# Optimization experiments

Measured on AMD Instinct MI355X. Metric: run time of the kernel, lower is better.

The kernel has to match this reference:

```python
import jax, jax.numpy as jnp
import numpy as np

N, E = 50000, 800000
IN_DIM, HEADS, OUT_DIM = 128, 4, 32
NEG_SLOPE = 0.2
EPS = 1e-16


def setup_inputs() -> dict:
    key = jax.random.key(0)
    k = jax.random.split(key, 6)
    x = jax.random.normal(k[0], (N, IN_DIM), dtype=jnp.float32)
    edge_index = jax.random.randint(k[1], (2, E), 0, N, dtype=jnp.int64)
    # xavier-uniform-ish params
    lim_w = float(np.sqrt(6.0 / (IN_DIM + HEADS * OUT_DIM)))
    W = jax.random.uniform(k[2], (HEADS * OUT_DIM, IN_DIM), minval=-lim_w, maxval=lim_w, dtype=jnp.float32)
    lim_a = float(np.sqrt(6.0 / (1 + HEADS * OUT_DIM)))
    att_src = jax.random.uniform(k[3], (1, HEADS, OUT_DIM), minval=-lim_a, maxval=lim_a, dtype=jnp.float32)
    att_dst = jax.random.uniform(k[4], (1, HEADS, OUT_DIM), minval=-lim_a, maxval=lim_a, dtype=jnp.float32)
    bias = jnp.zeros((HEADS * OUT_DIM,), dtype=jnp.float32)
    return {"x": x, "edge_index": edge_index, "W": W, "att_src": att_src, "att_dst": att_dst, "bias": bias}


def reference(x, edge_index, W, att_src, att_dst, bias):
    n = x.shape[0]
    h = (x @ W.T).reshape(n, HEADS, OUT_DIM)           # (N,H,D)
    src, dst = edge_index[0], edge_index[1]
    a_src = jnp.sum(h * att_src, axis=-1)              # (N,H)
    a_dst = jnp.sum(h * att_dst, axis=-1)              # (N,H)
    alpha = a_src[src] + a_dst[dst]                    # (E,H)
    alpha = jax.nn.leaky_relu(alpha, NEG_SLOPE)
    # segment (per-dst) softmax over edges, per head
    m = jax.ops.segment_max(alpha, dst, num_segments=n)   # (N,H)
    ex = jnp.exp(alpha - m[dst])
    s = jax.ops.segment_sum(ex, dst, num_segments=n)      # (N,H)
    alpha = ex / (s[dst] + EPS)                            # (E,H)
    # dropout p=0 (eval) -> identity
    msg = h[src] * alpha[..., None]                        # (E,H,D)
    out = jax.ops.segment_sum(msg, dst, num_segments=n)    # (N,H,D)
    out = out.reshape(n, HEADS * OUT_DIM) + bias
    alpha_pooled = alpha.mean(axis=-1)                     # (E,)
    return out, alpha_pooled
```

## Files before the change

### kernel.cpp

```cpp
#include <hip/hip_runtime.h>

#define NNODES 50000
#define NEDGES 800000
#define HD 128
#define NEG 0.2f
#define MTILE 64
#define LDW 136
#define MAXD 64
#define GEMMB ((NNODES + MTILE - 1) / MTILE)
#define NBINS 196
#define CAP 5120
#define GST 16
#define ABLK ((NEDGES + 2047) / 2048)

typedef __attribute__((ext_vector_type(8))) short short8;
typedef __attribute__((ext_vector_type(4))) float floatx4;

static __device__ inline unsigned short f2bf(float f) {
    unsigned u = __float_as_uint(f);
    return (unsigned short)((u + 0x7FFF + ((u >> 16) & 1)) >> 16);
}
static __device__ inline float bf2f(unsigned short u) {
    return __uint_as_float(((unsigned)u) << 16);
}
static __device__ inline float lrelu_exp(float a) {
    a = (a > 0.f) ? a : NEG * a;
    return __expf(a);
}

__global__ __launch_bounds__(256, 4) void gat_main(
    const float* __restrict__ x, const float* __restrict__ W,
    const float* __restrict__ att_src, const float* __restrict__ att_dst,
    const int* __restrict__ ei,
    unsigned short* __restrict__ h, float* __restrict__ asrc,
    float* __restrict__ adst, int* __restrict__ gcnt, int2* __restrict__ cbuf)
{
    __shared__ unsigned short Wl[128 * LDW];
    const int t = threadIdx.x;

    if (blockIdx.x >= GEMMB) {
        int* hist = (int*)Wl;
        int* boff = hist + 256;
        const int e0 = (blockIdx.x - GEMMB) * 2048 + t * 8;
        const bool act = (e0 < NEDGES);
        int4 s0 = make_int4(0, 0, 0, 0), s1 = s0, d0 = s0, d1 = s0;
        if (act) {
            s0 = *(const int4*)(ei + e0);
            s1 = *(const int4*)(ei + e0 + 4);
            d0 = *(const int4*)(ei + NEDGES + e0);
            d1 = *(const int4*)(ei + NEDGES + e0 + 4);
        }
        hist[t] = 0;
        __syncthreads();
        if (act) {
            atomicAdd(&hist[d0.x >> 8], 1); atomicAdd(&hist[d0.y >> 8], 1);
            atomicAdd(&hist[d0.z >> 8], 1); atomicAdd(&hist[d0.w >> 8], 1);
            atomicAdd(&hist[d1.x >> 8], 1); atomicAdd(&hist[d1.y >> 8], 1);
            atomicAdd(&hist[d1.z >> 8], 1); atomicAdd(&hist[d1.w >> 8], 1);
        }
        __syncthreads();
        if (t < NBINS && hist[t] > 0)
            boff[t] = atomicAdd(&gcnt[t * GST], hist[t]);
        __syncthreads();
        if (act) {
            int ss[8] = {s0.x, s0.y, s0.z, s0.w, s1.x, s1.y, s1.z, s1.w};
            int dd[8] = {d0.x, d0.y, d0.z, d0.w, d1.x, d1.y, d1.z, d1.w};
#pragma unroll
            for (int j = 0; j < 8; j++) {
                int b = dd[j] >> 8;
                int slot = atomicAdd(&boff[b], 1);
                cbuf[(size_t)b * CAP + slot] =
                    make_int2(((dd[j] & 255) << 16) | ss[j], e0 + j);
            }
        }
        return;
    }

    const int rowBase = blockIdx.x * MTILE;

    for (int idx = t * 8; idx < 128 * 128; idx += 2048) {
        int r = idx >> 7, c = idx & 127;
        float4 v0 = *(const float4*)(W + idx);
        float4 v1 = *(const float4*)(W + idx + 4);
        short8 u;
        u[0] = (short)f2bf(v0.x); u[1] = (short)f2bf(v0.y);
        u[2] = (short)f2bf(v0.z); u[3] = (short)f2bf(v0.w);
        u[4] = (short)f2bf(v1.x); u[5] = (short)f2bf(v1.y);
        u[6] = (short)f2bf(v1.z); u[7] = (short)f2bf(v1.w);
        *(short8*)(Wl + r * LDW + c) = u;
    }

    const int wave = t >> 6;
    const int lane = t & 63;
    const int c16  = lane & 15;
    const int quad = lane >> 4;
    const int xr   = rowBase + wave * 16 + c16;
    short8 av[4];
#pragma unroll
    for (int kc = 0; kc < 4; kc++) {
        float4 v0 = make_float4(0.f, 0.f, 0.f, 0.f);
        float4 v1 = v0;
        if (xr < NNODES) {
            const float* p = x + (size_t)xr * 128 + kc * 32 + quad * 8;
            v0 = *(const float4*)p;
            v1 = *(const float4*)(p + 4);
        }
        short8 u;
        u[0] = (short)f2bf(v0.x); u[1] = (short)f2bf(v0.y);
        u[2] = (short)f2bf(v0.z); u[3] = (short)f2bf(v0.w);
        u[4] = (short)f2bf(v1.x); u[5] = (short)f2bf(v1.y);
        u[6] = (short)f2bf(v1.z); u[7] = (short)f2bf(v1.w);
        av[kc] = u;
    }
    __syncthreads();

    floatx4 acc[8];
#pragma unroll
    for (int nt = 0; nt < 8; nt++) acc[nt] = (floatx4)(0.f);

#pragma unroll
    for (int kc = 0; kc < 4; kc++) {
#pragma unroll
        for (int nt = 0; nt < 8; nt++) {
            short8 bv = *(const short8*)(Wl + (nt * 16 + c16) * LDW + kc * 32 + quad * 8);
            acc[nt] = __builtin_amdgcn_mfma_f32_16x16x32_bf16(av[kc], bv, acc[nt], 0, 0, 0);
        }
    }

    float As[8], Ad[8];
#pragma unroll
    for (int nt = 0; nt < 8; nt++) {
        As[nt] = att_src[nt * 16 + c16];
        Ad[nt] = att_dst[nt * 16 + c16];
    }
#pragma unroll
    for (int r = 0; r < 4; r++) {
        const int gr = rowBase + wave * 16 + quad * 4 + r;
#pragma unroll
        for (int hh = 0; hh < 4; hh++) {
            float ps = acc[2 * hh][r] * As[2 * hh] + acc[2 * hh + 1][r] * As[2 * hh + 1];
            float pd = acc[2 * hh][r] * Ad[2 * hh] + acc[2 * hh + 1][r] * Ad[2 * hh + 1];
#pragma unroll
            for (int m = 8; m >= 1; m >>= 1) {
                ps += __shfl_xor(ps, m, 64);
                pd += __shfl_xor(pd, m, 64);
            }
            if (c16 == 0 && gr < NNODES) {
                asrc[gr * 4 + hh] = ps;
                adst[gr * 4 + hh] = pd;
            }
        }
    }

    __syncthreads();
#pragma unroll
    for (int r = 0; r < 4; r++) {
        const int lr = wave * 16 + quad * 4 + r;
#pragma unroll
        for (int nt = 0; nt < 8; nt++)
            Wl[lr * LDW + nt * 16 + c16] = f2bf(acc[nt][r]);
    }
    __syncthreads();
    for (int idx = t * 8; idx < MTILE * 128; idx += 2048) {
        int r = idx >> 7, c = idx & 127;
        int g = rowBase + r;
        if (g < NNODES)
            *(short8*)(h + (size_t)g * HD + c) = *(const short8*)(Wl + r * LDW + c);
    }
}

__global__ __launch_bounds__(1024) void gat_bin(
    const int* __restrict__ gcnt, const int2* __restrict__ cbuf,
    int* __restrict__ coff, int2* __restrict__ csr)
{
    __shared__ int sh[256];
    __shared__ int hist[256];
    const int t = threadIdx.x;
    const int b = blockIdx.x;
    const int c_b = gcnt[b * GST];

    int v = 0;
    if (t < 256) {
        v = (t < NBINS) ? gcnt[t * GST] : 0;
        sh[t] = v;
        hist[t] = 0;
    }
    __syncthreads();
    for (int off = 1; off < 256; off <<= 1) {
        int u = (t < 256 && t >= off) ? sh[t - off] : 0;
        __syncthreads();
        if (t < 256) sh[t] += u;
        __syncthreads();
    }
    const int binbase = sh[b] - c_b;

    for (int i = t; i < c_b; i += 1024)
        atomicAdd(&hist[(cbuf[(size_t)b * CAP + i].x >> 16) & 255], 1);
    __syncthreads();

    int hv = 0;
    if (t < 256) { hv = hist[t]; sh[t] = hv; }
    __syncthreads();
    for (int off = 1; off < 256; off <<= 1) {
        int u = (t < 256 && t >= off) ? sh[t - off] : 0;
        __syncthreads();
        if (t < 256) sh[t] += u;
        __syncthreads();
    }
    if (t < 256) {
        int ex = sh[t] - hv;
        int n = b * 256 + t;
        if (n < NNODES) coff[n] = binbase + ex;
        hist[t] = ex;
    }
    if (b == 0 && t == 0) coff[NNODES] = NEDGES;
    __syncthreads();

    for (int i = t; i < c_b; i += 1024) {
        int2 ew = cbuf[(size_t)b * CAP + i];
        int fine = (ew.x >> 16) & 255;
        int slot = atomicAdd(&hist[fine], 1);
        csr[binbase + slot] = make_int2(ew.x & 0xffff, ew.y);
    }
}

__global__ __launch_bounds__(256) void gat_node(
    const int* __restrict__ coff, const int2* __restrict__ csr_se,
    const float* __restrict__ asrc, const float* __restrict__ adst,
    const unsigned short* __restrict__ h, const float* __restrict__ bias,
    float* __restrict__ out, float* __restrict__ apool)
{
    __shared__ int   sh_src[8 * MAXD];
    __shared__ int   sh_eid[8 * MAXD];
    __shared__ float sh_w[8 * MAXD * 4];
    int t = threadIdx.x;
    int node8 = t >> 5;
    int n = blockIdx.x * 8 + node8;
    int k = t & 31;
    int head = k >> 3;
    int beg = coff[n], end = coff[n + 1];
    const float4 bn = *(const float4*)(adst + n * 4);

    float4 sum = make_float4(0.f, 0.f, 0.f, 0.f);
    for (int j = beg + k; j < end; j += 32) {
        int2 se = csr_se[j];
        float4 a = *(const float4*)(asrc + se.x * 4);
        float4 wv;
        wv.x = lrelu_exp(a.x + bn.x);
        wv.y = lrelu_exp(a.y + bn.y);
        wv.z = lrelu_exp(a.z + bn.z);
        wv.w = lrelu_exp(a.w + bn.w);
        sum.x += wv.x; sum.y += wv.y; sum.z += wv.z; sum.w += wv.w;
        int i = j - beg;
        if (i < MAXD) {
            sh_src[node8 * MAXD + i] = se.x;
            sh_eid[node8 * MAXD + i] = se.y;
            *(float4*)(sh_w + (node8 * MAXD + i) * 4) = wv;
        }
    }
#pragma unroll
    for (int m = 16; m >= 1; m >>= 1) {
        sum.x += __shfl_xor(sum.x, m, 64);
        sum.y += __shfl_xor(sum.y, m, 64);
        sum.z += __shfl_xor(sum.z, m, 64);
        sum.w += __shfl_xor(sum.w, m, 64);
    }
    float rs[4];
    rs[0] = 1.f / (sum.x + 1e-16f);
    rs[1] = 1.f / (sum.y + 1e-16f);
    rs[2] = 1.f / (sum.z + 1e-16f);
    rs[3] = 1.f / (sum.w + 1e-16f);
    const float rsel = rs[head];
    __syncthreads();

    const int cnt = end - beg;
    const int lim = (cnt < MAXD) ? cnt : MAXD;
    const int base = node8 * MAXD;
    float4 acc = *(const float4*)(bias + k * 4);
    float4 acc2 = make_float4(0.f, 0.f, 0.f, 0.f);
    int i = 0;
    for (; i + 4 <= lim; i += 4) {
        int s0 = sh_src[base + i];
        int s1 = sh_src[base + i + 1];
        int s2 = sh_src[base + i + 2];
        int s3 = sh_src[base + i + 3];
        float w0 = sh_w[(base + i) * 4 + head] * rsel;
        float w1 = sh_w[(base + i + 1) * 4 + head] * rsel;
        float w2 = sh_w[(base + i + 2) * 4 + head] * rsel;
        float w3 = sh_w[(base + i + 3) * 4 + head] * rsel;
        ushort4 u0 = *(const ushort4*)(h + (size_t)s0 * HD + k * 4);
        ushort4 u1 = *(const ushort4*)(h + (size_t)s1 * HD + k * 4);
        ushort4 u2 = *(const ushort4*)(h + (size_t)s2 * HD + k * 4);
        ushort4 u3 = *(const ushort4*)(h + (size_t)s3 * HD + k * 4);
        acc.x  = fmaf(bf2f(u0.x), w0, acc.x);
        acc.y  = fmaf(bf2f(u0.y), w0, acc.y);
        acc.z  = fmaf(bf2f(u0.z), w0, acc.z);
        acc.w  = fmaf(bf2f(u0.w), w0, acc.w);
        acc2.x = fmaf(bf2f(u1.x), w1, acc2.x);
        acc2.y = fmaf(bf2f(u1.y), w1, acc2.y);
        acc2.z = fmaf(bf2f(u1.z), w1, acc2.z);
        acc2.w = fmaf(bf2f(u1.w), w1, acc2.w);
        acc.x  = fmaf(bf2f(u2.x), w2, acc.x);
        acc.y  = fmaf(bf2f(u2.y), w2, acc.y);
        acc.z  = fmaf(bf2f(u2.z), w2, acc.z);
        acc.w  = fmaf(bf2f(u2.w), w2, acc.w);
        acc2.x = fmaf(bf2f(u3.x), w3, acc2.x);
        acc2.y = fmaf(bf2f(u3.y), w3, acc2.y);
        acc2.z = fmaf(bf2f(u3.z), w3, acc2.z);
        acc2.w = fmaf(bf2f(u3.w), w3, acc2.w);
    }
    for (; i < lim; i++) {
        int s0 = sh_src[base + i];
        float w0 = sh_w[(base + i) * 4 + head] * rsel;
        ushort4 u0 = *(const ushort4*)(h + (size_t)s0 * HD + k * 4);
        acc.x = fmaf(bf2f(u0.x), w0, acc.x);
        acc.y = fmaf(bf2f(u0.y), w0, acc.y);
        acc.z = fmaf(bf2f(u0.z), w0, acc.z);
        acc.w = fmaf(bf2f(u0.w), w0, acc.w);
    }
    for (int j = beg + MAXD; j < end; j++) {
        int2 se = csr_se[j];
        float4 a = *(const float4*)(asrc + se.x * 4);
        float w4[4];
        w4[0] = lrelu_exp(a.x + bn.x);
        w4[1] = lrelu_exp(a.y + bn.y);
        w4[2] = lrelu_exp(a.z + bn.z);
        w4[3] = lrelu_exp(a.w + bn.w);
        float w0 = w4[head] * rsel;
        ushort4 u0 = *(const ushort4*)(h + (size_t)se.x * HD + k * 4);
        acc.x = fmaf(bf2f(u0.x), w0, acc.x);
        acc.y = fmaf(bf2f(u0.y), w0, acc.y);
        acc.z = fmaf(bf2f(u0.z), w0, acc.z);
        acc.w = fmaf(bf2f(u0.w), w0, acc.w);
        if (k == 0)
            apool[se.y] = 0.25f * (w4[0] * rs[0] + w4[1] * rs[1] +
                                   w4[2] * rs[2] + w4[3] * rs[3]);
    }
    acc.x += acc2.x; acc.y += acc2.y; acc.z += acc2.z; acc.w += acc2.w;
    *(float4*)(out + (size_t)n * HD + k * 4) = acc;

    for (int i2 = k; i2 < lim; i2 += 32) {
        float4 w = *(const float4*)(sh_w + (base + i2) * 4);
        apool[sh_eid[base + i2]] =
            0.25f * (w.x * rs[0] + w.y * rs[1] + w.z * rs[2] + w.w * rs[3]);
    }
}

extern "C" void kernel_launch(void* const* d_in, const int* in_sizes, int n_in,
                              void* d_out, int out_size, void* d_ws, size_t ws_size,
                              hipStream_t stream)
{
    const float* x       = (const float*)d_in[0];
    const int*   ei      = (const int*)d_in[1];
    const float* W       = (const float*)d_in[2];
    const float* att_src = (const float*)d_in[3];
    const float* att_dst = (const float*)d_in[4];
    const float* bias    = (const float*)d_in[5];

    float* out   = (float*)d_out;
    float* apool = out + (size_t)NNODES * HD;

    unsigned short* h = (unsigned short*)d_ws;
    float* asrc = (float*)(h + (size_t)NNODES * HD);
    float* adst = asrc + NNODES * 4;
    int*   gcnt = (int*)(adst + NNODES * 4);
    int*   coff = gcnt + NBINS * GST;
    int2*  cbuf = (int2*)(coff + NNODES + 4);
    int2*  csr  = cbuf + (size_t)NBINS * CAP;

    hipMemsetAsync(gcnt, 0, (size_t)NBINS * GST * sizeof(int), stream);

    gat_main<<<GEMMB + ABLK, 256, 0, stream>>>(
        x, W, att_src, att_dst, ei, h, asrc, adst, gcnt, cbuf);
    gat_bin<<<NBINS, 1024, 0, stream>>>(gcnt, cbuf, coff, csr);
    gat_node<<<NNODES / 8, 256, 0, stream>>>(
        coff, csr, asrc, adst, h, bias, out, apool);
}
```

Before: 157.6 us.

## Fuse CSR bin sort into node aggregation and compute alpha pooling per edge

Removes the separate gat_bin kernel and global CSR array. Each fused block now re-reads its coarse bin bucket, sorts the 64 destination nodes it owns into shared memory, and aggregates directly from there. The pooled attention output moves to a new edge-parallel kernel that recomputes each edge's weight from saved per-node reciprocal sums, so edge ids no longer need to be stored. The coarse bucket payload shrinks to one int per edge. Each bucket is now scanned by four blocks, the new kernel adds a pass over the edges, and edges past ECAP per quarter bin are silently dropped.

After: 166.5 us. +5.6%, slower.

```diff
diff --git a/kernel.cpp b/kernel.cpp
--- a/kernel.cpp
+++ b/kernel.cpp
@@ -6,12 +6,12 @@
 #define NEG 0.2f
 #define MTILE 64
 #define LDW 136
-#define MAXD 64
 #define GEMMB ((NNODES + MTILE - 1) / MTILE)
 #define NBINS 196
 #define CAP 5120
 #define GST 16
 #define ABLK ((NEDGES + 2047) / 2048)
+#define ECAP 1536
 
 typedef __attribute__((ext_vector_type(8))) short short8;
 typedef __attribute__((ext_vector_type(4))) float floatx4;
@@ -33,7 +33,7 @@
     const float* __restrict__ att_src, const float* __restrict__ att_dst,
     const int* __restrict__ ei,
     unsigned short* __restrict__ h, float* __restrict__ asrc,
-    float* __restrict__ adst, int* __restrict__ gcnt, int2* __restrict__ cbuf)
+    float* __restrict__ adst, int* __restrict__ gcnt, int* __restrict__ cbuf)
 {
     __shared__ unsigned short Wl[128 * LDW];
     const int t = threadIdx.x;
@@ -69,8 +69,7 @@
             for (int j = 0; j < 8; j++) {
                 int b = dd[j] >> 8;
                 int slot = atomicAdd(&boff[b], 1);
-                cbuf[(size_t)b * CAP + slot] =
-                    make_int2(((dd[j] & 255) << 16) | ss[j], e0 + j);
+                cbuf[(size_t)b * CAP + slot] = ((dd[j] & 255) << 16) | ss[j];
             }
         }
         return;
@@ -169,181 +168,171 @@
     }
 }
 
-__global__ __launch_bounds__(1024) void gat_bin(
-    const int* __restrict__ gcnt, const int2* __restrict__ cbuf,
-    int* __restrict__ coff, int2* __restrict__ csr)
-{
-    __shared__ int sh[256];
-    __shared__ int hist[256];
-    const int t = threadIdx.x;
-    const int b = blockIdx.x;
-    const int c_b = gcnt[b * GST];
-
-    int v = 0;
-    if (t < 256) {
-        v = (t < NBINS) ? gcnt[t * GST] : 0;
-        sh[t] = v;
-        hist[t] = 0;
-    }
-    __syncthreads();
-    for (int off = 1; off < 256; off <<= 1) {
-        int u = (t < 256 && t >= off) ? sh[t - off] : 0;
-        __syncthreads();
-        if (t < 256) sh[t] += u;
-        __syncthreads();
-    }
-    const int binbase = sh[b] - c_b;
-
-    for (int i = t; i < c_b; i += 1024)
-        atomicAdd(&hist[(cbuf[(size_t)b * CAP + i].x >> 16) & 255], 1);
-    __syncthreads();
-
-    int hv = 0;
-    if (t < 256) { hv = hist[t]; sh[t] = hv; }
-    __syncthreads();
-    for (int off = 1; off < 256; off <<= 1) {
-        int u = (t < 256 && t >= off) ? sh[t - off] : 0;
-        __syncthreads();
-        if (t < 256) sh[t] += u;
-        __syncthreads();
-    }
-    if (t < 256) {
-        int ex = sh[t] - hv;
-        int n = b * 256 + t;
-        if (n < NNODES) coff[n] = binbase + ex;
-        hist[t] = ex;
-    }
-    if (b == 0 && t == 0) coff[NNODES] = NEDGES;
-    __syncthreads();
-
-    for (int i = t; i < c_b; i += 1024) {
-        int2 ew = cbuf[(size_t)b * CAP + i];
-        int fine = (ew.x >> 16) & 255;
-        int slot = atomicAdd(&hist[fine], 1);
-        csr[binbase + slot] = make_int2(ew.x & 0xffff, ew.y);
-    }
-}
-
-__global__ __launch_bounds__(256) void gat_node(
-    const int* __restrict__ coff, const int2* __restrict__ csr_se,
+__global__ __launch_bounds__(256) void gat_fuse(
+    const int* __restrict__ gcnt, const int* __restrict__ cbuf,
     const float* __restrict__ asrc, const float* __restrict__ adst,
     const unsigned short* __restrict__ h, const float* __restrict__ bias,
-    float* __restrict__ out, float* __restrict__ apool)
-{
-    __shared__ int   sh_src[8 * MAXD];
-    __shared__ int   sh_eid[8 * MAXD];
-    __shared__ float sh_w[8 * MAXD * 4];
-    int t = threadIdx.x;
-    int node8 = t >> 5;
-    int n = blockIdx.x * 8 + node8;
-    int k = t & 31;
-    int head = k >> 3;
-    int beg = coff[n], end = coff[n + 1];
-    const float4 bn = *(const float4*)(adst + n * 4);
-
-    float4 sum = make_float4(0.f, 0.f, 0.f, 0.f);
-    for (int j = beg + k; j < end; j += 32) {
-        int2 se = csr_se[j];
-        float4 a = *(const float4*)(asrc + se.x * 4);
-        float4 wv;
-        wv.x = lrelu_exp(a.x + bn.x);
-        wv.y = lrelu_exp(a.y + bn.y);
-        wv.z = lrelu_exp(a.z + bn.z);
-        wv.w = lrelu_exp(a.w + bn.w);
-        sum.x += wv.x; sum.y += wv.y; sum.z += wv.z; sum.w += wv.w;
-        int i = j - beg;
-        if (i < MAXD) {
-            sh_src[node8 * MAXD + i] = se.x;
-            sh_eid[node8 * MAXD + i] = se.y;
-            *(float4*)(sh_w + (node8 * MAXD + i) * 4) = wv;
-        }
-    }
-#pragma unroll
-    for (int m = 16; m >= 1; m >>= 1) {
-        sum.x += __shfl_xor(sum.x, m, 64);
-        sum.y += __shfl_xor(sum.y, m, 64);
-        sum.z += __shfl_xor(sum.z, m, 64);
-        sum.w += __shfl_xor(sum.w, m, 64);
-    }
-    float rs[4];
-    rs[0] = 1.f / (sum.x + 1e-16f);
-    rs[1] = 1.f / (sum.y + 1e-16f);
-    rs[2] = 1.f / (sum.z + 1e-16f);
-    rs[3] = 1.f / (sum.w + 1e-16f);
-    const float rsel = rs[head];
-    __syncthreads();
-
-    const int cnt = end - beg;
-    const int lim = (cnt < MAXD) ? cnt : MAXD;
-    const int base = node8 * MAXD;
-    float4 acc = *(const float4*)(bias + k * 4);
-    float4 acc2 = make_float4(0.f, 0.f, 0.f, 0.f);
-    int i = 0;
-    for (; i + 4 <= lim; i += 4) {
-        int s0 = sh_src[base + i];
-        int s1 = sh_src[base + i + 1];
-        int s2 = sh_src[base + i + 2];
-        int s3 = sh_src[base + i + 3];
-        float w0 = sh_w[(base + i) * 4 + head] * rsel;
-        float w1 = sh_w[(base + i + 1) * 4 + head] * rsel;
-        float w2 = sh_w[(base + i + 2) * 4 + head] * rsel;
-        float w3 = sh_w[(base + i + 3) * 4 + head] * rsel;
-        ushort4 u0 = *(const ushort4*)(h + (size_t)s0 * HD + k * 4);
-        ushort4 u1 = *(const ushort4*)(h + (size_t)s1 * HD + k * 4);
-        ushort4 u2 = *(const ushort4*)(h + (size_t)s2 * HD + k * 4);
-        ushort4 u3 = *(const ushort4*)(h + (size_t)s3 * HD + k * 4);
-        acc.x  = fmaf(bf2f(u0.x), w0, acc.x);
-        acc.y  = fmaf(bf2f(u0.y), w0, acc.y);
-        acc.z  = fmaf(bf2f(u0.z), w0, acc.z);
-        acc.w  = fmaf(bf2f(u0.w), w0, acc.w);
-        acc2.x = fmaf(bf2f(u1.x), w1, acc2.x);
-        acc2.y = fmaf(bf2f(u1.y), w1, acc2.y);
-        acc2.z = fmaf(bf2f(u1.z), w1, acc2.z);
-        acc2.w = fmaf(bf2f(u1.w), w1, acc2.w);
-        acc.x  = fmaf(bf2f(u2.x), w2, acc.x);
-        acc.y  = fmaf(bf2f(u2.y), w2, acc.y);
-        acc.z  = fmaf(bf2f(u2.z), w2, acc.z);
-        acc.w  = fmaf(bf2f(u2.w), w2, acc.w);
-        acc2.x = fmaf(bf2f(u3.x), w3, acc2.x);
-        acc2.y = fmaf(bf2f(u3.y), w3, acc2.y);
-        acc2.z = fmaf(bf2f(u3.z), w3, acc2.z);
-        acc2.w = fmaf(bf2f(u3.w), w3, acc2.w);
-    }
-    for (; i < lim; i++) {
-        int s0 = sh_src[base + i];
-        float w0 = sh_w[(base + i) * 4 + head] * rsel;
-        ushort4 u0 = *(const ushort4*)(h + (size_t)s0 * HD + k * 4);
-        acc.x = fmaf(bf2f(u0.x), w0, acc.x);
-        acc.y = fmaf(bf2f(u0.y), w0, acc.y);
-        acc.z = fmaf(bf2f(u0.z), w0, acc.z);
-        acc.w = fmaf(bf2f(u0.w), w0, acc.w);
-    }
-    for (int j = beg + MAXD; j < end; j++) {
-        int2 se = csr_se[j];
-        float4 a = *(const float4*)(asrc + se.x * 4);
-        float w4[4];
-        w4[0] = lrelu_exp(a.x + bn.x);
-        w4[1] = lrelu_exp(a.y + bn.y);
-        w4[2] = lrelu_exp(a.z + bn.z);
-        w4[3] = lrelu_exp(a.w + bn.w);
-        float w0 = w4[head] * rsel;
-        ushort4 u0 = *(const ushort4*)(h + (size_t)se.x * HD + k * 4);
-        acc.x = fmaf(bf2f(u0.x), w0, acc.x);
-        acc.y = fmaf(bf2f(u0.y), w0, acc.y);
-        acc.z = fmaf(bf2f(u0.z), w0, acc.z);
-        acc.w = fmaf(bf2f(u0.w), w0, acc.w);
-        if (k == 0)
-            apool[se.y] = 0.25f * (w4[0] * rs[0] + w4[1] * rs[1] +
-                                   w4[2] * rs[2] + w4[3] * rs[3]);
-    }
-    acc.x += acc2.x; acc.y += acc2.y; acc.z += acc2.z; acc.w += acc2.w;
-    *(float4*)(out + (size_t)n * HD + k * 4) = acc;
-
-    for (int i2 = k; i2 < lim; i2 += 32) {
-        float4 w = *(const float4*)(sh_w + (base + i2) * 4);
-        apool[sh_eid[base + i2]] =
-            0.25f * (w.x * rs[0] + w.y * rs[1] + w.z * rs[2] + w.w * rs[3]);
-    }
+    float* __restrict__ out, float* __restrict__ rsumr)
+{
+    __shared__ unsigned short eb[ECAP];
+    __shared__ float sh_w[ECAP * 4];
+    __shared__ int hist[64], run[64], beg[65];
+    const int t = threadIdx.x;
+    const int b = blockIdx.x >> 2;
+    const int q = blockIdx.x & 3;
+    const int c_b = gcnt[b * GST];
+    const size_t wbase = (size_t)b * CAP;
+
+    if (t < 64) hist[t] = 0;
+    __syncthreads();
+    for (int i = t; i < c_b; i += 256) {
+        int e = cbuf[wbase + i];
+        int f = (e >> 16) & 255;
+        if ((f >> 6) == q) atomicAdd(&hist[f & 63], 1);
+    }
+    __syncthreads();
+    if (t < 64) {
+        int v = hist[t];
+        int s = v;
+#pragma unroll
+        for (int off = 1; off < 64; off <<= 1) {
+            int u = __shfl_up(s, off, 64);
+            if (t >= off) s += u;
+        }
+        beg[t] = s - v;
+        run[t] = s - v;
+        if (t == 63) beg[64] = s;
+    }
+    __syncthreads();
+    for (int i = t; i < c_b; i += 256) {
+        int e = cbuf[wbase + i];
+        int f = (e >> 16) & 255;
+        if ((f >> 6) == q) {
+            int slot = atomicAdd(&run[f & 63], 1);
+            if (slot < ECAP) eb[slot] = (unsigned short)(e & 0xFFFF);
+        }
+    }
+    __syncthreads();
+
+    const int grp  = t >> 5;
+    const int k    = t & 31;
+    const int head = k >> 3;
+    const float4 bias4 = *(const float4*)(bias + k * 4);
+
+    for (int ii = 0; ii < 8; ii++) {
+        const int local = grp * 8 + ii;
+        const int n = b * 256 + q * 64 + local;
+        int eB = beg[local], eE = beg[local + 1];
+        if (eE > ECAP) eE = ECAP;
+        if (eB > ECAP) eB = ECAP;
+
+        float4 bn = make_float4(0.f, 0.f, 0.f, 0.f);
+        if (n < NNODES) bn = *(const float4*)(adst + n * 4);
+
+        float4 sum = make_float4(0.f, 0.f, 0.f, 0.f);
+        for (int j = eB + k; j < eE; j += 32) {
+            int s = eb[j];
+            float4 a = *(const float4*)(asrc + s * 4);
+            float4 wv;
+            wv.x = lrelu_exp(a.x + bn.x);
+            wv.y = lrelu_exp(a.y + bn.y);
+            wv.z = lrelu_exp(a.z + bn.z);
+            wv.w = lrelu_exp(a.w + bn.w);
+            sum.x += wv.x; sum.y += wv.y; sum.z += wv.z; sum.w += wv.w;
+            *(float4*)(sh_w + j * 4) = wv;
+        }
+#pragma unroll
+        for (int m = 16; m >= 1; m >>= 1) {
+            sum.x += __shfl_xor(sum.x, m, 64);
+            sum.y += __shfl_xor(sum.y, m, 64);
+            sum.z += __shfl_xor(sum.z, m, 64);
+            sum.w += __shfl_xor(sum.w, m, 64);
+        }
+        float rs[4];
+        rs[0] = 1.f / (sum.x + 1e-16f);
+        rs[1] = 1.f / (sum.y + 1e-16f);
+        rs[2] = 1.f / (sum.z + 1e-16f);
+        rs[3] = 1.f / (sum.w + 1e-16f);
+        if (n < NNODES && k == 0) {
+            float4 r4 = make_float4(rs[0], rs[1], rs[2], rs[3]);
+            *(float4*)(rsumr + n * 4) = r4;
+        }
+        const float rsel = rs[head];
+
+        float4 acc = bias4;
+        float4 acc2 = make_float4(0.f, 0.f, 0.f, 0.f);
+        int i = eB;
+        for (; i + 4 <= eE; i += 4) {
+            int s0 = eb[i];
+            int s1 = eb[i + 1];
+            int s2 = eb[i + 2];
+            int s3 = eb[i + 3];
+            float w0 = sh_w[i * 4 + head] * rsel;
+            float w1 = sh_w[(i + 1) * 4 + head] * rsel;
+            float w2 = sh_w[(i + 2) * 4 + head] * rsel;
+            float w3 = sh_w[(i + 3) * 4 + head] * rsel;
+            ushort4 u0 = *(const ushort4*)(h + (size_t)s0 * HD + k * 4);
+            ushort4 u1 = *(const ushort4*)(h + (size_t)s1 * HD + k * 4);
+            ushort4 u2 = *(const ushort4*)(h + (size_t)s2 * HD + k * 4);
+            ushort4 u3 = *(const ushort4*)(h + (size_t)s3 * HD + k * 4);
+            acc.x  = fmaf(bf2f(u0.x), w0, acc.x);
+            acc.y  = fmaf(bf2f(u0.y), w0, acc.y);
+            acc.z  = fmaf(bf2f(u0.z), w0, acc.z);
+            acc.w  = fmaf(bf2f(u0.w), w0, acc.w);
+            acc2.x = fmaf(bf2f(u1.x), w1, acc2.x);
+            acc2.y = fmaf(bf2f(u1.y), w1, acc2.y);
+            acc2.z = fmaf(bf2f(u1.z), w1, acc2.z);
+            acc2.w = fmaf(bf2f(u1.w), w1, acc2.w);
+            acc.x  = fmaf(bf2f(u2.x), w2, acc.x);
+            acc.y  = fmaf(bf2f(u2.y), w2, acc.y);
+            acc.z  = fmaf(bf2f(u2.z), w2, acc.z);
+            acc.w  = fmaf(bf2f(u2.w), w2, acc.w);
+            acc2.x = fmaf(bf2f(u3.x), w3, acc2.x);
+            acc2.y = fmaf(bf2f(u3.y), w3, acc2.y);
+            acc2.z = fmaf(bf2f(u3.z), w3, acc2.z);
+            acc2.w = fmaf(bf2f(u3.w), w3, acc2.w);
+        }
+        for (; i < eE; i++) {
+            int s0 = eb[i];
+            float w0 = sh_w[i * 4 + head] * rsel;
+            ushort4 u0 = *(const ushort4*)(h + (size_t)s0 * HD + k * 4);
+            acc.x = fmaf(bf2f(u0.x), w0, acc.x);
+            acc.y = fmaf(bf2f(u0.y), w0, acc.y);
+            acc.z = fmaf(bf2f(u0.z), w0, acc.z);
+            acc.w = fmaf(bf2f(u0.w), w0, acc.w);
+        }
+        acc.x += acc2.x; acc.y += acc2.y; acc.z += acc2.z; acc.w += acc2.w;
+        if (n < NNODES)
+            *(float4*)(out + (size_t)n * HD + k * 4) = acc;
+    }
+}
+
+static __device__ inline float apool1(
+    int s, int d, const float* __restrict__ asrc,
+    const float* __restrict__ adst, const float* __restrict__ rsumr)
+{
+    float4 a = *(const float4*)(asrc + s * 4);
+    float4 b = *(const float4*)(adst + d * 4);
+    float4 r = *(const float4*)(rsumr + d * 4);
+    return 0.25f * (lrelu_exp(a.x + b.x) * r.x + lrelu_exp(a.y + b.y) * r.y +
+                    lrelu_exp(a.z + b.z) * r.z + lrelu_exp(a.w + b.w) * r.w);
+}
+
+__global__ __launch_bounds__(256) void gat_apool(
+    const int* __restrict__ ei, const float* __restrict__ asrc,
+    const float* __restrict__ adst, const float* __restrict__ rsumr,
+    float* __restrict__ apool)
+{
+    int e0 = (blockIdx.x * 256 + threadIdx.x) * 4;
+    if (e0 >= NEDGES) return;
+    int4 s = *(const int4*)(ei + e0);
+    int4 d = *(const int4*)(ei + NEDGES + e0);
+    float4 r;
+    r.x = apool1(s.x, d.x, asrc, adst, rsumr);
+    r.y = apool1(s.y, d.y, asrc, adst, rsumr);
+    r.z = apool1(s.z, d.z, asrc, adst, rsumr);
+    r.w = apool1(s.w, d.w, asrc, adst, rsumr);
+    *(float4*)(apool + e0) = r;
 }
 
 extern "C" void kernel_launch(void* const* d_in, const int* in_sizes, int n_in,
@@ -361,18 +350,18 @@
     float* apool = out + (size_t)NNODES * HD;
 
     unsigned short* h = (unsigned short*)d_ws;
-    float* asrc = (float*)(h + (size_t)NNODES * HD);
-    float* adst = asrc + NNODES * 4;
-    int*   gcnt = (int*)(adst + NNODES * 4);
-    int*   coff = gcnt + NBINS * GST;
-    int2*  cbuf = (int2*)(coff + NNODES + 4);
-    int2*  csr  = cbuf + (size_t)NBINS * CAP;
+    float* asrc  = (float*)(h + (size_t)NNODES * HD);
+    float* adst  = asrc + NNODES * 4;
+    float* rsumr = adst + NNODES * 4;
+    int*   gcnt  = (int*)(rsumr + NNODES * 4);
+    int*   cbuf  = gcnt + NBINS * GST;
 
     hipMemsetAsync(gcnt, 0, (size_t)NBINS * GST * sizeof(int), stream);
 
     gat_main<<<GEMMB + ABLK, 256, 0, stream>>>(
         x, W, att_src, att_dst, ei, h, asrc, adst, gcnt, cbuf);
-    gat_bin<<<NBINS, 1024, 0, stream>>>(gcnt, cbuf, coff, csr);
-    gat_node<<<NNODES / 8, 256, 0, stream>>>(
-        coff, csr, asrc, adst, h, bias, out, apool);
-}
+    gat_fuse<<<NBINS * 4, 256, 0, stream>>>(
+        gcnt, cbuf, asrc, adst, h, bias, out, rsumr);
+    gat_apool<<<(NEDGES / 4 + 255) / 256, 256, 0, stream>>>(
+        ei, asrc, adst, rsumr, apool);
+}
```
